# Kernel optimization log

Hardware: AMD Instinct MI355X
Metric: run time of the kernel (lower is better)

## Reference

```python
import jax, jax.numpy as jnp
import numpy as np

N_NODES = 10000
W_DIM = 512
N_EDGES = 200000


def setup_inputs() -> dict:
    key = jax.random.key(0)
    k1, k2, k3 = jax.random.split(key, 3)
    z_drug = jax.random.normal(k1, (N_NODES, W_DIM), dtype=jnp.float32)
    # glorot-style init for the bilinear weight
    glorot_std = jnp.sqrt(2.0 / (W_DIM + W_DIM)).astype(jnp.float32)
    weight = jax.random.normal(k2, (W_DIM, W_DIM), dtype=jnp.float32) * glorot_std
    batch_edges = jax.random.randint(k3, (2, N_EDGES), 0, N_NODES, dtype=jnp.int64)
    return {"z_drug": z_drug, "weight": weight, "batch_edges": batch_edges}


def reference(z_drug, weight, batch_edges):
    # edge_type == 'drug_drug': both endpoints come from the drug table.
    row_embed = z_drug[batch_edges[0]]  # [E, d]
    col_embed = z_drug[batch_edges[1]]  # [E, d]
    # score_e = row_e @ W @ col_e  == diag((Z1 W) Z2^T) without the N x N blowup
    score = jnp.einsum('ed,df,ef->e', row_embed, weight, col_embed)
    return jax.nn.sigmoid(score)  # is_sigmoid=True default
```

## Files before the change

kernel.cpp:

```cpp
#include <hip/hip_runtime.h>
#include <math.h>

#define DIM     512
#define NNODES  10000
#define NEDGES  200000
#define MPAD    10240
#define NMB     160
#define NGRP    5
#define NB      (NGRP * NNODES)
#define SCAN_N  49
#define GEMM_GRID (NMB * 4)

#define HIST_BLK   50
#define SCAN_BASE  50
#define SCAT_BASE  99
#define SCAT_N     98
#define GEMM_BASE  197
#define FUSE_GRID  (GEMM_BASE + GEMM_GRID)

using floatx4 = __attribute__((ext_vector_type(4))) float;
using half8   = __attribute__((ext_vector_type(8))) _Float16;
using half2v  = __attribute__((ext_vector_type(2))) _Float16;

__device__ inline float dot2acc(half2v a, half2v b, float c) {
#if __has_builtin(__builtin_amdgcn_fdot2)
    return __builtin_amdgcn_fdot2(a, b, c, false);
#else
    return fmaf((float)a[0], (float)b[0], fmaf((float)a[1], (float)b[1], c));
#endif
}

__device__ inline int aload(const int* p) {
    return __hip_atomic_load(p, __ATOMIC_RELAXED, __HIP_MEMORY_SCOPE_AGENT);
}
__device__ inline void astore(int* p, int v) {
    __hip_atomic_store(p, v, __ATOMIC_RELAXED, __HIP_MEMORY_SCOPE_AGENT);
}
__device__ inline void waitflag(int* f, int target) {
    while (__hip_atomic_load(f, __ATOMIC_RELAXED, __HIP_MEMORY_SCOPE_AGENT) < target)
        __builtin_amdgcn_s_sleep(8);
    __atomic_signal_fence(__ATOMIC_ACQUIRE);
}
__device__ inline void signal(int* f) {
    __atomic_signal_fence(__ATOMIC_RELEASE);
    __hip_atomic_fetch_add(f, 1, __ATOMIC_RELAXED, __HIP_MEMORY_SCOPE_AGENT);
}

#define PREP_ZBLK 2560
__global__ __launch_bounds__(256) void prep(const float* __restrict__ Z,
                                            const float* __restrict__ W,
                                            _Float16* __restrict__ Zh16,
                                            _Float16* __restrict__ Wh16t,
                                            int* __restrict__ counts,
                                            int* __restrict__ flags) {
    const int b = blockIdx.x;
    const int t = threadIdx.x;

    if (b == 0 && t < 4) flags[t] = 0;

    if (b < 196) {
        int i = b * 256 + t;
        if (i < NB) counts[i] = 0;
    }

    if (b < PREP_ZBLK) {
        const int idx8 = (b * 256 + t) * 8;
        const int m = idx8 >> 9;
        float x[8];
        if (m < NNODES) {
            float4 v0 = *(const float4*)(Z + idx8);
            float4 v1 = *(const float4*)(Z + idx8 + 4);
            x[0]=v0.x; x[1]=v0.y; x[2]=v0.z; x[3]=v0.w;
            x[4]=v1.x; x[5]=v1.y; x[6]=v1.z; x[7]=v1.w;
        } else {
            #pragma unroll
            for (int j = 0; j < 8; ++j) x[j] = 0.f;
        }
        half8 h;
        #pragma unroll
        for (int j = 0; j < 8; ++j) h[j] = (_Float16)x[j];
        *(half8*)(Zh16 + idx8) = h;
    } else {
        __shared__ float tile[64][65];
        const int wb = b - PREP_ZBLK;
        const int kb = (wb >> 3) * 64;
        const int nb = (wb & 7) * 64;
        const int kk = t >> 2;
        const int ch = t & 3;

        const float* src = W + (size_t)(kb + kk) * DIM + nb + ch * 16;
        #pragma unroll
        for (int q = 0; q < 4; ++q) {
            float4 v = *(const float4*)(src + q * 4);
            tile[kk][ch * 16 + q * 4 + 0] = v.x;
            tile[kk][ch * 16 + q * 4 + 1] = v.y;
            tile[kk][ch * 16 + q * 4 + 2] = v.z;
            tile[kk][ch * 16 + q * 4 + 3] = v.w;
        }
        __syncthreads();

        const int nn = kk;
        half8 h0, h1;
        #pragma unroll
        for (int i = 0; i < 8; ++i) h0[i] = (_Float16)tile[ch * 16 + i][nn];
        #pragma unroll
        for (int i = 0; i < 8; ++i) h1[i] = (_Float16)tile[ch * 16 + 8 + i][nn];
        _Float16* d = Wh16t + (size_t)(nb + nn) * DIM + kb + ch * 16;
        *(half8*)(d)     = h0;
        *(half8*)(d + 8) = h1;
    }
}

__global__ __launch_bounds__(256, 3) void gemm_sort(
        const _Float16* __restrict__ Zh16,
        const _Float16* __restrict__ Wh16t,
        _Float16* __restrict__ ZWh,
        const int* __restrict__ eidx,
        int* __restrict__ counts,
        int* __restrict__ cursor,
        int* __restrict__ blksum,
        unsigned* __restrict__ keys,
        unsigned short* __restrict__ rows16,
        int* __restrict__ flags)
{
    __shared__ _Float16 Abuf[2][2 * 64 * 32];
    __shared__ _Float16 Bbuf[2][2 * 128 * 32];
    __shared__ int wsum[4];
    __shared__ int sbase;

    const int t   = threadIdx.x;
    const int bid = blockIdx.x;

    if (bid >= GEMM_BASE) {
        const int s8  = bid - GEMM_BASE;
        const int cxd = bid & 7;
        const int rr  = s8 >> 3;
        const int mg  = (rr >> 2) * 8 + cxd;
        const int m0  = mg * 64;
        const int n0  = (rr & 3) * 128;

        const int l  = t & 63;
        const int w  = t >> 6;
        const int wn = w * 32;
        const int lm = l & 15;
        const int lq = l >> 4;
        const unsigned wbase = (unsigned)(t & 192);

        floatx4 acc[4][2] = {};

        auto stage = [&](int buf, int k0) {
            #pragma unroll
            for (int p = 0; p < 2; ++p) {
                const int s   = p * 256 + t;
                const int kk  = s >> 8;
                const int row = (s >> 2) & 63;
                const int ch  = s & 3;
                const _Float16* src = Zh16 + (size_t)(m0 + row) * DIM + k0 + kk * 32 + ch * 8;
                __builtin_amdgcn_global_load_lds(
                    (const __attribute__((address_space(1))) void*)src,
                    (__attribute__((address_space(3))) void*)&Abuf[buf][(p * 256 + wbase) * 8],
                    16, 0, 0);
            }
            #pragma unroll
            for (int p = 0; p < 4; ++p) {
                const int s   = p * 256 + t;
                const int kk  = s >> 9;
                const int row = (s >> 2) & 127;
                const int ch  = s & 3;
                const _Float16* src = Wh16t + (size_t)(n0 + row) * DIM + k0 + kk * 32 + ch * 8;
                __builtin_amdgcn_global_load_lds(
                    (const __attribute__((address_space(1))) void*)src,
                    (__attribute__((address_space(3))) void*)&Bbuf[buf][(p * 256 + wbase) * 8],
                    16, 0, 0);
            }
        };

        stage(0, 0);
        __syncthreads();

        for (int s = 0; s < 8; ++s) {
            const int buf = s & 1;
            if (s < 7) stage(buf ^ 1, (s + 1) * 64);

            #pragma unroll
            for (int kk = 0; kk < 2; ++kk) {
                half8 aF[4], bF[2];
                #pragma unroll
                for (int i = 0; i < 4; ++i)
                    aF[i] = *(const half8*)&Abuf[buf][kk * 2048 + (16 * i + lm) * 32 + lq * 8];
                #pragma unroll
                for (int j = 0; j < 2; ++j)
                    bF[j] = *(const half8*)&Bbuf[buf][kk * 4096 + (wn + 16 * j + lm) * 32 + lq * 8];

                #pragma unroll
                for (int i = 0; i < 4; ++i)
                    #pragma unroll
                    for (int j = 0; j < 2; ++j)
                        acc[i][j] = __builtin_amdgcn_mfma_f32_16x16x32_f16(aF[i], bF[j], acc[i][j], 0, 0, 0);
            }
            __syncthreads();
        }

        #pragma unroll
        for (int i = 0; i < 4; ++i)
            #pragma unroll
            for (int j = 0; j < 2; ++j)
                #pragma unroll
                for (int r = 0; r < 4; ++r) {
                    const int gm = m0 + 16 * i + lq * 4 + r;
                    const int gn = n0 + wn + 16 * j + lm;
                    if (gm < NNODES)
                        ZWh[(size_t)gm * DIM + gn] = (_Float16)acc[i][j][r];
                }
        return;
    }

    if (bid < HIST_BLK) {
        for (int e = bid * 256 + t; e < NEDGES; e += HIST_BLK * 256) {
            int r = eidx[e];
            int c = eidx[NEDGES + e];
            atomicAdd(&counts[(c >> 11) * NNODES + r], 1);
        }
        __syncthreads();
        if (t == 0) signal(&flags[0]);
        return;
    }

    if (bid < SCAT_BASE) {
        const int b = bid - SCAN_BASE;
        const int lane = t & 63;
        const int wv   = t >> 6;

        if (t == 0) waitflag(&flags[0], HIST_BLK);
        __syncthreads();

        const int base = b * 1024 + t * 4;
        int v0 = 0, v1 = 0, v2 = 0, v3 = 0;
        if (base + 3 < NB) {
            v0 = aload(counts + base);
            v1 = aload(counts + base + 1);
            v2 = aload(counts + base + 2);
            v3 = aload(counts + base + 3);
        } else {
            if (base     < NB) v0 = aload(counts + base);
            if (base + 1 < NB) v1 = aload(counts + base + 1);
            if (base + 2 < NB) v2 = aload(counts + base + 2);
        }
        const int ts = v0 + v1 + v2 + v3;
        int incl = ts;
        #pragma unroll
        for (int off = 1; off < 64; off <<= 1) {
            int u = __shfl_up(incl, off, 64);
            if (lane >= off) incl += u;
        }
        if (lane == 63) wsum[wv] = incl;
        __syncthreads();
        int wb = 0;
        #pragma unroll
        for (int k = 0; k < 4; ++k) if (k < wv) wb += wsum[k];
        const int ex   = wb + incl - ts;
        const int pre0 = ex;
        const int pre1 = ex + v0;
        const int pre2 = pre1 + v1;
        const int pre3 = pre2 + v2;
        if (t == 255) astore(blksum + b, wb + incl);
        __syncthreads();
        if (t == 0) { signal(&flags[1]); waitflag(&flags[1], SCAN_N); }
        __syncthreads();

        if (t < 64) {
            int v = (t < b) ? aload(blksum + t) : 0;
            #pragma unroll
            for (int off = 32; off > 0; off >>= 1)
                v += __shfl_xor(v, off, 64);
            if (t == 0) sbase = v;
        }
        __syncthreads();
        const int b0 = sbase;

        if (base + 3 < NB) {
            astore(cursor + base,     b0 + pre0);
            astore(cursor + base + 1, b0 + pre1);
            astore(cursor + base + 2, b0 + pre2);
            astore(cursor + base + 3, b0 + pre3);
        } else {
            if (base     < NB) astore(cursor + base,     b0 + pre0);
            if (base + 1 < NB) astore(cursor + base + 1, b0 + pre1);
            if (base + 2 < NB) astore(cursor + base + 2, b0 + pre2);
        }
        __syncthreads();
        if (t == 0) signal(&flags[2]);
        return;
    }

    {
        if (t == 0) waitflag(&flags[2], SCAN_N);
        __syncthreads();

        for (int e = (bid - SCAT_BASE) * 256 + t; e < NEDGES; e += SCAT_N * 256) {
            int r = eidx[e];
            int c = eidx[NEDGES + e];
            int pos = atomicAdd(&cursor[(c >> 11) * NNODES + r], 1);
            keys[pos]   = ((unsigned)c << 18) | (unsigned)e;
            rows16[pos] = (unsigned short)r;
        }
    }
}

__global__ __launch_bounds__(256) void edge_score_f(const _Float16* __restrict__ ZWh,
                                                    const _Float16* __restrict__ Zh,
                                                    const unsigned* __restrict__ keys,
                                                    const unsigned short* __restrict__ rows16,
                                                    float* __restrict__ out) {
    const int t    = threadIdx.x;
    const int wgid = blockIdx.x * 4 + (t >> 6);
    const int lane = t & 63;
    const int gq   = lane >> 4;
    const int sl   = lane & 15;

    const int ii = wgid * 4 + gq;
    const unsigned k = keys[ii];
    const int c = (int)(k >> 18);
    const int r = (int)rows16[ii];

    const _Float16* rp = ZWh + (size_t)r * DIM + sl * 32;
    const _Float16* cp = Zh  + (size_t)c * DIM + sl * 32;

    half8 ra0 = *(const half8*)(rp);
    half8 ra1 = *(const half8*)(rp + 8);
    half8 ra2 = *(const half8*)(rp + 16);
    half8 ra3 = *(const half8*)(rp + 24);
    half8 c0  = *(const half8*)(cp);
    half8 c1  = *(const half8*)(cp + 8);
    half8 c2  = *(const half8*)(cp + 16);
    half8 c3  = *(const half8*)(cp + 24);

    float s = 0.f;
    #pragma unroll
    for (int d = 0; d < 4; ++d) {
        s = dot2acc((half2v){ra0[2*d], ra0[2*d+1]}, (half2v){c0[2*d], c0[2*d+1]}, s);
        s = dot2acc((half2v){ra1[2*d], ra1[2*d+1]}, (half2v){c1[2*d], c1[2*d+1]}, s);
        s = dot2acc((half2v){ra2[2*d], ra2[2*d+1]}, (half2v){c2[2*d], c2[2*d+1]}, s);
        s = dot2acc((half2v){ra3[2*d], ra3[2*d+1]}, (half2v){c3[2*d], c3[2*d+1]}, s);
    }

    s += __shfl_xor(s, 1, 64);
    s += __shfl_xor(s, 2, 64);
    s += __shfl_xor(s, 4, 64);
    s += __shfl_xor(s, 8, 64);

    if (sl == 0)
        out[k & 0x3FFFFu] = 1.0f / (1.0f + expf(-s));
}

#define GTM 128
#define GTN 64
#define GTK 16
#define LDA 132
#define LDB 68

__global__ __launch_bounds__(256) void gemm_zw(const float* __restrict__ A,
                                               const float* __restrict__ B,
                                               float* __restrict__ C) {
    __shared__ float As[GTK * LDA];
    __shared__ float Bs[GTK * LDB];

    const int t  = threadIdx.x;
    const int m0 = blockIdx.x * GTM;
    const int n0 = blockIdx.y * GTN;
    const int tx = t & 15;
    const int ty = t >> 4;

    float acc[8][4] = {};

    for (int k0 = 0; k0 < DIM; k0 += GTK) {
        #pragma unroll
        for (int p = 0; p < 2; ++p) {
            int f  = t + p * 256;
            int mm = f >> 2;
            int kq = f & 3;
            int m  = m0 + mm;
            float4 v = make_float4(0.f, 0.f, 0.f, 0.f);
            if (m < NNODES)
                v = *(const float4*)(A + (size_t)m * DIM + k0 + kq * 4);
            As[(kq * 4 + 0) * LDA + mm] = v.x;
            As[(kq * 4 + 1) * LDA + mm] = v.y;
            As[(kq * 4 + 2) * LDA + mm] = v.z;
            As[(kq * 4 + 3) * LDA + mm] = v.w;
        }
        {
            int kb = t >> 4, n4 = t & 15;
            *(float4*)&Bs[kb * LDB + n4 * 4] =
                *(const float4*)(B + (size_t)(k0 + kb) * DIM + n0 + n4 * 4);
        }
        __syncthreads();

        #pragma unroll
        for (int kk = 0; kk < GTK; ++kk) {
            float4 a0 = *(const float4*)&As[kk * LDA + ty * 8];
            float4 a1 = *(const float4*)&As[kk * LDA + ty * 8 + 4];
            float4 b  = *(const float4*)&Bs[kk * LDB + tx * 4];
            float av[8] = {a0.x, a0.y, a0.z, a0.w, a1.x, a1.y, a1.z, a1.w};
            float bv[4] = {b.x, b.y, b.z, b.w};
            #pragma unroll
            for (int i = 0; i < 8; ++i)
                #pragma unroll
                for (int j = 0; j < 4; ++j)
                    acc[i][j] = fmaf(av[i], bv[j], acc[i][j]);
        }
        __syncthreads();
    }

    #pragma unroll
    for (int i = 0; i < 8; ++i) {
        int m = m0 + ty * 8 + i;
        if (m < NNODES)
            *(float4*)(C + (size_t)m * DIM + n0 + tx * 4) =
                make_float4(acc[i][0], acc[i][1], acc[i][2], acc[i][3]);
    }
}

__global__ __launch_bounds__(256) void edge_score(const float* __restrict__ ZW,
                                                  const float* __restrict__ Z,
                                                  const int* __restrict__ eidx,
                                                  float* __restrict__ out) {
    const int e    = blockIdx.x * 4 + (threadIdx.x >> 6);
    const int lane = threadIdx.x & 63;

    const int r = eidx[e];
    const int c = eidx[NEDGES + e];

    const float4* pr = (const float4*)(ZW + (size_t)r * DIM);
    const float4* pc = (const float4*)(Z  + (size_t)c * DIM);

    float4 a0 = pr[lane * 2 + 0];
    float4 a1 = pr[lane * 2 + 1];
    float4 b0 = pc[lane * 2 + 0];
    float4 b1 = pc[lane * 2 + 1];

    float s = a0.x * b0.x;
    s = fmaf(a0.y, b0.y, s);
    s = fmaf(a0.z, b0.z, s);
    s = fmaf(a0.w, b0.w, s);
    s = fmaf(a1.x, b1.x, s);
    s = fmaf(a1.y, b1.y, s);
    s = fmaf(a1.z, b1.z, s);
    s = fmaf(a1.w, b1.w, s);

    #pragma unroll
    for (int off = 32; off > 0; off >>= 1)
        s += __shfl_xor(s, off, 64);

    if (lane == 0)
        out[e] = 1.0f / (1.0f + expf(-s));
}

extern "C" void kernel_launch(void* const* d_in, const int* in_sizes, int n_in,
                              void* d_out, int out_size, void* d_ws, size_t ws_size,
                              hipStream_t stream) {
    const float* Z  = (const float*)d_in[0];
    const float* W  = (const float*)d_in[1];
    const int*   EI = (const int*)d_in[2];
    float* out = (float*)d_out;

    char* p = (char*)d_ws;
    _Float16* ZWh   = (_Float16*)p;  p += (size_t)MPAD * DIM * 2;
    _Float16* Zh16  = (_Float16*)p;  p += (size_t)MPAD * DIM * 2;
    _Float16* Wh16t = (_Float16*)p;  p += (size_t)DIM * DIM * 2;
    int* counts  = (int*)p;          p += (size_t)NB * 4;
    int* cursor  = (int*)p;          p += (size_t)NB * 4;
    int* blksum  = (int*)p;          p += (size_t)SCAN_N * 4;
    unsigned* keys = (unsigned*)p;   p += (size_t)NEDGES * 4;
    unsigned short* rows16 = (unsigned short*)p; p += (size_t)NEDGES * 2;
    int* flags = (int*)p;            p += 4 * 4;
    const size_t need_full = (size_t)(p - (char*)d_ws);

    if (ws_size >= need_full) {
        prep<<<PREP_ZBLK + 64, 256, 0, stream>>>(Z, W, Zh16, Wh16t, counts, flags);
        gemm_sort<<<FUSE_GRID, 256, 0, stream>>>(Zh16, Wh16t, ZWh, EI, counts,
                                                 cursor, blksum, keys, rows16, flags);
        edge_score_f<<<NEDGES / 16, 256, 0, stream>>>(ZWh, Zh16, keys, rows16, out);
    } else {
        float* ZW = (float*)d_ws;
        dim3 g1((NNODES + GTM - 1) / GTM, DIM / GTN);
        gemm_zw<<<g1, 256, 0, stream>>>(Z, W, ZW);
        edge_score<<<NEDGES / 4, 256, 0, stream>>>(ZW, Z, EI, out);
    }
}
```

Measured before the change: 135.4 us.

## Prefetch two K-stages ahead with explicit vmcnt waits in GEMM loop

```diff
diff --git a/kernel.cpp b/kernel.cpp
--- a/kernel.cpp
+++ b/kernel.cpp
@@ -21,6 +21,8 @@
 using floatx4 = __attribute__((ext_vector_type(4))) float;
 using half8   = __attribute__((ext_vector_type(8))) _Float16;
 using half2v  = __attribute__((ext_vector_type(2))) _Float16;
+
+template <int N> struct IC { static constexpr int v = N; };
 
 __device__ inline float dot2acc(half2v a, half2v b, float c) {
 #if __has_builtin(__builtin_amdgcn_fdot2)
@@ -176,30 +178,46 @@
         };
 
         stage(0, 0);
-        __syncthreads();
-
-        for (int s = 0; s < 8; ++s) {
-            const int buf = s & 1;
-            if (s < 7) stage(buf ^ 1, (s + 1) * 64);
-
+        stage(1, 64);
+
+        auto step = [&](auto Sc) {
+            constexpr int S   = decltype(Sc)::v;
+            constexpr int buf = S & 1;
+            if constexpr (S < 7) asm volatile("s_waitcnt vmcnt(6)" ::: "memory");
+            else                 asm volatile("s_waitcnt vmcnt(0)" ::: "memory");
+            __builtin_amdgcn_sched_barrier(0);
+            __builtin_amdgcn_s_barrier();
+            __builtin_amdgcn_sched_barrier(0);
+
+            half8 aF[2][4], bF[2][2];
             #pragma unroll
             for (int kk = 0; kk < 2; ++kk) {
-                half8 aF[4], bF[2];
                 #pragma unroll
                 for (int i = 0; i < 4; ++i)
-                    aF[i] = *(const half8*)&Abuf[buf][kk * 2048 + (16 * i + lm) * 32 + lq * 8];
+                    aF[kk][i] = *(const half8*)&Abuf[buf][kk * 2048 + (16 * i + lm) * 32 + lq * 8];
                 #pragma unroll
                 for (int j = 0; j < 2; ++j)
-                    bF[j] = *(const half8*)&Bbuf[buf][kk * 4096 + (wn + 16 * j + lm) * 32 + lq * 8];
-
+                    bF[kk][j] = *(const half8*)&Bbuf[buf][kk * 4096 + (wn + 16 * j + lm) * 32 + lq * 8];
+            }
+            asm volatile("s_waitcnt lgkmcnt(0)" ::: "memory");
+            __builtin_amdgcn_sched_barrier(0);
+            __builtin_amdgcn_s_barrier();
+            __builtin_amdgcn_sched_barrier(0);
+
+            if constexpr (S < 6) stage(buf, (S + 2) * 64);
+
+            #pragma unroll
+            for (int kk = 0; kk < 2; ++kk)
                 #pragma unroll
                 for (int i = 0; i < 4; ++i)
                     #pragma unroll
                     for (int j = 0; j < 2; ++j)
-                        acc[i][j] = __builtin_amdgcn_mfma_f32_16x16x32_f16(aF[i], bF[j], acc[i][j], 0, 0, 0);
-            }
-            __syncthreads();
-        }
+                        acc[i][j] = __builtin_amdgcn_mfma_f32_16x16x32_f16(
+                            aF[kk][i], bF[kk][j], acc[i][j], 0, 0, 0);
+        };
+
+        step(IC<0>{}); step(IC<1>{}); step(IC<2>{}); step(IC<3>{});
+        step(IC<4>{}); step(IC<5>{}); step(IC<6>{}); step(IC<7>{});
 
         #pragma unroll
         for (int i = 0; i < 4; ++i)
```

Result: no change. 135.6 us (+0.1%).
